# Optimization experiments

Hardware: AMD Instinct MI355X
Metric: run time of the kernel (lower is better)

Reference implementation:

```python
import jax, jax.numpy as jnp
import numpy as np

D_MODEL = 1024
NUM_HEADS = 16
HEAD_DIM = D_MODEL // NUM_HEADS


def setup_inputs() -> dict:
    key = jax.random.key(0)
    ks = jax.random.split(key, 9)
    B, S = 2, 2048
    s = 1.0 / np.sqrt(D_MODEL)
    return {
        "x": jax.random.normal(ks[0], (B, S, D_MODEL), dtype=jnp.float32),
        "Wq": jax.random.normal(ks[1], (D_MODEL, D_MODEL), dtype=jnp.float32) * s,
        "bq": jnp.zeros((D_MODEL,), dtype=jnp.float32),
        "Wk": jax.random.normal(ks[2], (D_MODEL, D_MODEL), dtype=jnp.float32) * s,
        "bk": jnp.zeros((D_MODEL,), dtype=jnp.float32),
        "Wv": jax.random.normal(ks[3], (D_MODEL, D_MODEL), dtype=jnp.float32) * s,
        "bv": jnp.zeros((D_MODEL,), dtype=jnp.float32),
        "Wo": jax.random.normal(ks[4], (D_MODEL, D_MODEL), dtype=jnp.float32) * s,
        "bo": jnp.zeros((D_MODEL,), dtype=jnp.float32),
    }


def reference(x, Wq, bq, Wk, bk, Wv, bv, Wo, bo):
    B, S, _ = x.shape
    # linear projections then split heads: [B, S, D] -> [B, H, S, hd]
    def split_heads(t):
        return t.reshape(B, S, NUM_HEADS, HEAD_DIM).transpose(0, 2, 1, 3)
    q = split_heads(x @ Wq + bq)
    k = split_heads(x @ Wk + bk)
    v = split_heads(x @ Wv + bv)
    # scores: [B, H, S, S]
    scores = jnp.einsum('bhqd,bhkd->bhqk', q, k) / jnp.sqrt(
        jnp.asarray(HEAD_DIM, dtype=x.dtype))
    attn = jax.nn.softmax(scores, axis=-1)
    # dropout is identity in eval mode
    out = jnp.einsum('bhqk,bhkd->bhqd', attn, v)
    out = out.transpose(0, 2, 1, 3).reshape(B, S, D_MODEL)
    return out @ Wo + bo
```

## Files before the change

### kernel.cpp

```cpp
#include <hip/hip_runtime.h>

#define D_MODEL 1024
#define NHEAD 16
#define HD 64
#define BATCH 2
#define SEQ 2048

typedef unsigned short u16;
typedef unsigned int u32;
typedef __bf16 bf16x8 __attribute__((ext_vector_type(8)));
typedef unsigned short u16x8 __attribute__((ext_vector_type(8)));
typedef short s16x4 __attribute__((ext_vector_type(4)));
typedef float f32x4 __attribute__((ext_vector_type(4)));

#if defined(__has_builtin)
#if __has_builtin(__builtin_amdgcn_exp2f)
#define EXP2(x) __builtin_amdgcn_exp2f(x)
#else
#define EXP2(x) exp2f(x)
#endif
#else
#define EXP2(x) exp2f(x)
#endif

static __device__ __forceinline__ u16 f2bf(float f) {
    union { float f; unsigned u; } v; v.f = f;
    unsigned u = v.u;
    u += 0x7fffu + ((u >> 16) & 1u);
    return (u16)(u >> 16);
}

static __device__ __forceinline__ void gld_lds16(const void* g, void* l) {
    __builtin_amdgcn_global_load_lds(
        (const __attribute__((address_space(1))) void*)g,
        (__attribute__((address_space(3))) void*)l, 16, 0, 0);
}

static __device__ __forceinline__ bf16x8 pack_bf8(f32x4 a, f32x4 b) {
    union { float f; unsigned u; } a0, a1, a2, a3, b0, b1, b2, b3;
    a0.f = a[0]; a1.f = a[1]; a2.f = a[2]; a3.f = a[3];
    b0.f = b[0]; b1.f = b[1]; b2.f = b[2]; b3.f = b[3];
    union { unsigned u[4]; bf16x8 v; } r;
    r.u[0] = __builtin_amdgcn_perm(a1.u, a0.u, 0x07060302u);
    r.u[1] = __builtin_amdgcn_perm(a3.u, a2.u, 0x07060302u);
    r.u[2] = __builtin_amdgcn_perm(b1.u, b0.u, 0x07060302u);
    r.u[3] = __builtin_amdgcn_perm(b3.u, b2.u, 0x07060302u);
    return r.v;
}

__global__ __launch_bounds__(256) void k_convert(const float* __restrict__ x,
                                                 const float* __restrict__ wq,
                                                 const float* __restrict__ wk,
                                                 const float* __restrict__ wv,
                                                 const float* __restrict__ wo,
                                                 u16* __restrict__ xb,
                                                 u16* __restrict__ wt) {
    int z = blockIdx.z;
    if (z == 0) {
        int base = (blockIdx.y * 32 + blockIdx.x) * 256 + threadIdx.x;
#pragma unroll
        for (int p = 0; p < 4; p++) {
            int i = base + p * 262144;
            float4 v = ((const float4*)x)[i];
            ushort4 o = make_ushort4(f2bf(v.x), f2bf(v.y), f2bf(v.z), f2bf(v.w));
            ((ushort4*)xb)[i] = o;
        }
        return;
    }
    __shared__ u16 t[32][33];
    const float* W = z == 1 ? wq : z == 2 ? wk : z == 3 ? wv : wo;
    u16* dst = wt + (size_t)(z - 1) * (D_MODEL * D_MODEL);
    int tx = threadIdx.x & 31, ty = threadIdx.x >> 5;
    int n0 = blockIdx.x * 32, k0 = blockIdx.y * 32;
#pragma unroll
    for (int i = 0; i < 4; i++)
        t[ty + i * 8][tx] = f2bf(W[(size_t)(k0 + ty + i * 8) * D_MODEL + n0 + tx]);
    __syncthreads();
#pragma unroll
    for (int i = 0; i < 4; i++)
        dst[(size_t)(n0 + ty + i * 8) * D_MODEL + k0 + tx] = t[tx][ty + i * 8];
}

__global__ __launch_bounds__(256) void k_gemm(const u16* __restrict__ A,
                                              const u16* __restrict__ WtBase,
                                              const float* __restrict__ b0,
                                              const float* __restrict__ b1,
                                              const float* __restrict__ b2,
                                              u16* __restrict__ oq, u16* __restrict__ ok,
                                              u16* __restrict__ ov) {
    __shared__ u16 lA[2 * 128 * 32];
    __shared__ u16 lB[2 * 128 * 32];
    int tid = threadIdx.x, w = tid >> 6, l = tid & 63, lr = l & 15, lq = l >> 4;
    int z = blockIdx.z;
    const u16* Wt = WtBase + (size_t)z * (D_MODEL * D_MODEL);
    const float* bias = z == 0 ? b0 : z == 1 ? b1 : b2;
    float scale = (z == 0) ? (0.125f * 1.44269504088896340736f) : 1.0f;
    int fid2 = blockIdx.y * 8 + blockIdx.x;
    int swz = (fid2 & 7) * 32 + (fid2 >> 3);
    int bx = swz & 7, by = swz >> 3;
    int m0 = by * 128, n0 = bx * 128;
    int wm = (w >> 1) * 64, wn = (w & 1) * 64;
    f32x4 acc[4][4];
#pragma unroll
    for (int mi = 0; mi < 4; mi++)
#pragma unroll
        for (int ni = 0; ni < 4; ni++) acc[mi][ni] = (f32x4){0.f, 0.f, 0.f, 0.f};

    int ra = tid >> 2, ca = (tid & 3) * 8;
    const u16* Aba = A + (size_t)(m0 + ra) * D_MODEL + ca;
    const u16* Abb = A + (size_t)(m0 + 64 + ra) * D_MODEL + ca;
    const u16* Bba = Wt + (size_t)(n0 + ra) * D_MODEL + ca;
    const u16* Bbb = Wt + (size_t)(n0 + 64 + ra) * D_MODEL + ca;

    auto stage = [&](int kk, int buf) {
        gld_lds16(Aba + kk, &lA[buf * 4096 + w * 512]);
        gld_lds16(Abb + kk, &lA[buf * 4096 + 2048 + w * 512]);
        gld_lds16(Bba + kk, &lB[buf * 4096 + w * 512]);
        gld_lds16(Bbb + kk, &lB[buf * 4096 + 2048 + w * 512]);
    };

    stage(0, 0);
    __syncthreads();
    int cur = 0;
    for (int t = 0; t < 32; ++t) {
        if (t + 1 < 32) stage((t + 1) * 32, cur ^ 1);
        bf16x8 af[4], bf[4];
#pragma unroll
        for (int mi = 0; mi < 4; mi++)
            af[mi] = *(const bf16x8*)&lA[cur * 4096 + (wm + mi * 16 + lr) * 32 + lq * 8];
#pragma unroll
        for (int ni = 0; ni < 4; ni++)
            bf[ni] = *(const bf16x8*)&lB[cur * 4096 + (wn + ni * 16 + lr) * 32 + lq * 8];
        __builtin_amdgcn_s_setprio(1);
#pragma unroll
        for (int mi = 0; mi < 4; mi++)
#pragma unroll
            for (int ni = 0; ni < 4; ni++)
                acc[mi][ni] = __builtin_amdgcn_mfma_f32_16x16x32_bf16(
                    af[mi], bf[ni], acc[mi][ni], 0, 0, 0);
        __builtin_amdgcn_s_setprio(0);
        __syncthreads();
        cur ^= 1;
    }
#pragma unroll
    for (int mi = 0; mi < 4; mi++) {
#pragma unroll
        for (int ni = 0; ni < 4; ni++) {
            int col = n0 + wn + ni * 16 + lr;
            float bval = bias[col];
            int row0 = m0 + wm + mi * 16 + lq * 4;
            if (z == 2) {
                int b = row0 >> 11, s = row0 & 2047;
                int h = col >> 6, dd = col & 63;
                ushort4 pk;
                pk.x = f2bf(acc[mi][ni][0] + bval);
                pk.y = f2bf(acc[mi][ni][1] + bval);
                pk.z = f2bf(acc[mi][ni][2] + bval);
                pk.w = f2bf(acc[mi][ni][3] + bval);
                *(ushort4*)&ov[((size_t)(b * NHEAD + h) * HD + dd) * SEQ + s] = pk;
            } else {
#pragma unroll
                for (int r = 0; r < 4; r++) {
                    int row = row0 + r;
                    float val = (acc[mi][ni][r] + bval) * scale;
                    u16* op = z == 0 ? oq : ok;
                    int b = row >> 11, s = row & 2047, h = col >> 6, d = col & 63;
                    op[(((size_t)(b * NHEAD + h)) * SEQ + s) * HD + d] = f2bf(val);
                }
            }
        }
    }
}

__global__ __launch_bounds__(256) void k_gout(const u16* __restrict__ A,
                                              const u16* __restrict__ Wt,
                                              const float* __restrict__ bias,
                                              float* __restrict__ outf) {
    __shared__ u16 lA[2 * 64 * 32];
    __shared__ u16 lB[2 * 64 * 32];
    int tid = threadIdx.x, w = tid >> 6, l = tid & 63, lr = l & 15, lq = l >> 4;
    int fid = blockIdx.y * 16 + blockIdx.x;
    int swz = (fid & 7) * 128 + (fid >> 3);
    int bx = swz & 15, by = swz >> 4;
    int m0 = by * 64, n0 = bx * 64;
    int wm = (w >> 1) * 32, wn = (w & 1) * 32;
    f32x4 acc[2][2];
#pragma unroll
    for (int mi = 0; mi < 2; mi++)
#pragma unroll
        for (int ni = 0; ni < 2; ni++) acc[mi][ni] = (f32x4){0.f, 0.f, 0.f, 0.f};

    int ra = tid >> 2, ca = (tid & 3) * 8;
    const u16* Aba = A + (size_t)(m0 + ra) * D_MODEL + ca;
    const u16* Bba = Wt + (size_t)(n0 + ra) * D_MODEL + ca;

    auto stage = [&](int kk, int buf) {
        gld_lds16(Aba + kk, &lA[buf * 2048 + w * 512]);
        gld_lds16(Bba + kk, &lB[buf * 2048 + w * 512]);
    };

    stage(0, 0);
    __syncthreads();
    int cur = 0;
    for (int t = 0; t < 32; ++t) {
        if (t + 1 < 32) stage((t + 1) * 32, cur ^ 1);
        bf16x8 af[2], bf[2];
#pragma unroll
        for (int mi = 0; mi < 2; mi++)
            af[mi] = *(const bf16x8*)&lA[cur * 2048 + (wm + mi * 16 + lr) * 32 + lq * 8];
#pragma unroll
        for (int ni = 0; ni < 2; ni++)
            bf[ni] = *(const bf16x8*)&lB[cur * 2048 + (wn + ni * 16 + lr) * 32 + lq * 8];
        __builtin_amdgcn_s_setprio(1);
#pragma unroll
        for (int mi = 0; mi < 2; mi++)
#pragma unroll
            for (int ni = 0; ni < 2; ni++)
                acc[mi][ni] = __builtin_amdgcn_mfma_f32_16x16x32_bf16(
                    af[mi], bf[ni], acc[mi][ni], 0, 0, 0);
        __builtin_amdgcn_s_setprio(0);
        __syncthreads();
        cur ^= 1;
    }
#pragma unroll
    for (int mi = 0; mi < 2; mi++)
#pragma unroll
        for (int ni = 0; ni < 2; ni++) {
            int col = n0 + wn + ni * 16 + lr;
            float bval = bias[col];
#pragma unroll
            for (int r = 0; r < 4; r++) {
                int row = m0 + wm + mi * 16 + lq * 4 + r;
                outf[(size_t)row * D_MODEL + col] = acc[mi][ni][r] + bval;
            }
        }
}

static __device__ __forceinline__ int ksw(int row, int col) {
    return row * 64 + ((((col >> 3) ^ (row & 7)) << 3) | (col & 7));
}
static __device__ __forceinline__ int vsw(int row, int col) {
    return row * 128 + ((((col >> 3) ^ (row & 15)) << 3) | (col & 7));
}

__global__ __launch_bounds__(256) void k_attn(const u16* __restrict__ Q,
                                              const u16* __restrict__ K,
                                              const u16* __restrict__ VT,
                                              u16* __restrict__ part0,
                                              u16* __restrict__ part1,
                                              float* __restrict__ lsum, int nsplit) {
    __shared__ __align__(16) u16 lK[128 * 64];
    __shared__ __align__(16) u16 lVt[64 * 128];
    int tid = threadIdx.x, w = tid >> 6, l = tid & 63, lr = l & 15, lq = l >> 4;
    int bl = blockIdx.x;
    int qt = bl / (32 * nsplit);
    int rem = bl - qt * (32 * nsplit);
    int bh = rem / nsplit;
    int ks = rem - bh * nsplit;
    int qb = qt * 128 + w * 32;
    const u16* Qb = Q + (size_t)bh * SEQ * HD;
    const u16* Kb = K + (size_t)bh * SEQ * HD;
    const u16* VTb = VT + (size_t)bh * HD * SEQ;

    bf16x8 qf[2][2];
#pragma unroll
    for (int tq = 0; tq < 2; tq++)
#pragma unroll
        for (int kc = 0; kc < 2; kc++)
            qf[tq][kc] = *(const bf16x8*)&Qb[(size_t)(qb + tq * 16 + lr) * HD +
                                             kc * 32 + lq * 8];
    f32x4 o[2][4];
    f32x4 ol[2];
#pragma unroll
    for (int tq = 0; tq < 2; tq++) {
        ol[tq] = (f32x4){0.f, 0.f, 0.f, 0.f};
#pragma unroll
        for (int di = 0; di < 4; di++) o[tq][di] = (f32x4){0.f, 0.f, 0.f, 0.f};
    }
    union { u16 s[8]; bf16x8 v; } onev;
#pragma unroll
    for (int i = 0; i < 8; i++) onev.s[i] = 0x3F80;
    const bf16x8 vone8 = onev.v;

    int krow = tid >> 3, kch = tid & 7;
    int vrow = tid >> 4, vch = tid & 15;

    int nk = SEQ / nsplit;
    int jbeg = ks * nk, jend = jbeg + nk;

    u16x8 kreg[4], vreg[4];
#pragma unroll
    for (int p = 0; p < 4; p++) {
        kreg[p] = *(const u16x8*)&Kb[(size_t)(jbeg + p * 32 + krow) * HD + kch * 8];
        vreg[p] = *(const u16x8*)&VTb[(size_t)(p * 16 + vrow) * SEQ + jbeg + vch * 8];
    }

    for (int j0 = jbeg; j0 < jend; j0 += 128) {
        __syncthreads();
#pragma unroll
        for (int p = 0; p < 4; p++) {
            *(u16x8*)&lK[ksw(p * 32 + krow, kch * 8)] = kreg[p];
            *(u16x8*)&lVt[vsw(p * 16 + vrow, vch * 8)] = vreg[p];
        }
        __syncthreads();
        if (j0 + 128 < jend) {
            int jn = j0 + 128;
#pragma unroll
            for (int p = 0; p < 4; p++) {
                kreg[p] = *(const u16x8*)&Kb[(size_t)(jn + p * 32 + krow) * HD + kch * 8];
                vreg[p] = *(const u16x8*)&VTb[(size_t)(p * 16 + vrow) * SEQ + jn + vch * 8];
            }
        }

#pragma unroll
        for (int kh = 0; kh < 2; kh++) {
#pragma unroll
            for (int t2 = 0; t2 < 2; t2++) {
                int rA = kh * 64 + t2 * 32 + lr;
                int rB = rA + 16;
                bf16x8 kA0 = *(const bf16x8*)&lK[ksw(rA, lq * 8)];
                bf16x8 kA1 = *(const bf16x8*)&lK[ksw(rA, 32 + lq * 8)];
                bf16x8 kB0 = *(const bf16x8*)&lK[ksw(rB, lq * 8)];
                bf16x8 kB1 = *(const bf16x8*)&lK[ksw(rB, 32 + lq * 8)];
                f32x4 sA0 = (f32x4){0.f, 0.f, 0.f, 0.f};
                f32x4 sA1 = (f32x4){0.f, 0.f, 0.f, 0.f};
                f32x4 sB0 = (f32x4){0.f, 0.f, 0.f, 0.f};
                f32x4 sB1 = (f32x4){0.f, 0.f, 0.f, 0.f};
                __builtin_amdgcn_s_setprio(1);
                sA0 = __builtin_amdgcn_mfma_f32_16x16x32_bf16(kA0, qf[0][0], sA0, 0, 0, 0);
                sB0 = __builtin_amdgcn_mfma_f32_16x16x32_bf16(kB0, qf[0][0], sB0, 0, 0, 0);
                sA1 = __builtin_amdgcn_mfma_f32_16x16x32_bf16(kA0, qf[1][0], sA1, 0, 0, 0);
                sB1 = __builtin_amdgcn_mfma_f32_16x16x32_bf16(kB0, qf[1][0], sB1, 0, 0, 0);
                sA0 = __builtin_amdgcn_mfma_f32_16x16x32_bf16(kA1, qf[0][1], sA0, 0, 0, 0);
                sB0 = __builtin_amdgcn_mfma_f32_16x16x32_bf16(kB1, qf[0][1], sB0, 0, 0, 0);
                sA1 = __builtin_amdgcn_mfma_f32_16x16x32_bf16(kA1, qf[1][1], sA1, 0, 0, 0);
                sB1 = __builtin_amdgcn_mfma_f32_16x16x32_bf16(kB1, qf[1][1], sB1, 0, 0, 0);
                __builtin_amdgcn_s_setprio(0);
#pragma unroll
                for (int r = 0; r < 4; r++) {
                    sA0[r] = EXP2(sA0[r]);
                    sA1[r] = EXP2(sA1[r]);
                    sB0[r] = EXP2(sB0[r]);
                    sB1[r] = EXP2(sB1[r]);
                }
                bf16x8 pf0 = pack_bf8(sA0, sB0);
                bf16x8 pf1 = pack_bf8(sA1, sB1);
                __builtin_amdgcn_s_setprio(1);
                ol[0] = __builtin_amdgcn_mfma_f32_16x16x32_bf16(pf0, vone8, ol[0], 0, 0, 0);
                ol[1] = __builtin_amdgcn_mfma_f32_16x16x32_bf16(pf1, vone8, ol[1], 0, 0, 0);
#pragma unroll
                for (int di = 0; di < 4; di++) {
                    int vr = di * 16 + lr;
                    union { bf16x8 v; s16x4 h[2]; } vv;
                    vv.h[0] = *(const s16x4*)&lVt[vsw(vr, kh * 64 + t2 * 32 + lq * 4)];
                    vv.h[1] = *(const s16x4*)&lVt[vsw(vr, kh * 64 + t2 * 32 + 16 + lq * 4)];
                    o[0][di] = __builtin_amdgcn_mfma_f32_16x16x32_bf16(pf0, vv.v,
                                                                       o[0][di], 0, 0, 0);
                    o[1][di] = __builtin_amdgcn_mfma_f32_16x16x32_bf16(pf1, vv.v,
                                                                       o[1][di], 0, 0, 0);
                }
                __builtin_amdgcn_s_setprio(0);
            }
        }
    }
    int b = bh >> 4, h = bh & 15;
    if (nsplit == 1) {
#pragma unroll
        for (int tq = 0; tq < 2; tq++) {
#pragma unroll
            for (int di = 0; di < 4; di++)
#pragma unroll
                for (int r = 0; r < 4; r++) {
                    int qg = qb + tq * 16 + lq * 4 + r;
                    part0[((size_t)(b * SEQ + qg)) * D_MODEL + h * 64 + di * 16 + lr] =
                        f2bf(o[tq][di][r] / ol[tq][r]);
                }
        }
    } else {
        u16* pdst = (ks == 0) ? part0 : part1;
#pragma unroll
        for (int tq = 0; tq < 2; tq++)
#pragma unroll
            for (int di = 0; di < 4; di++)
#pragma unroll
                for (int r = 0; r < 4; r++) {
                    int qg = qb + tq * 16 + lq * 4 + r;
                    union { _Float16 h; u16 u; } cv;
                    cv.h = (_Float16)o[tq][di][r];
                    pdst[((size_t)(b * SEQ + qg)) * D_MODEL + h * 64 + di * 16 + lr] =
                        cv.u;
                }
        if (lr == 0) {
#pragma unroll
            for (int tq = 0; tq < 2; tq++)
#pragma unroll
                for (int r = 0; r < 4; r++) {
                    int qg = qb + tq * 16 + lq * 4 + r;
                    lsum[(ks * 32 + bh) * 2048 + qg] = ol[tq][r];
                }
        }
    }
}

__global__ __launch_bounds__(256) void k_combine(const u16* __restrict__ p0,
                                                 const u16* __restrict__ p1,
                                                 const float* __restrict__ lsum,
                                                 u16* __restrict__ dst) {
    int i = blockIdx.x * 256 + threadIdx.x;
    size_t a8 = (size_t)i * 8;
    int row = (int)(a8 >> 10);
    int col = (int)(a8 & 1023);
    int b = row >> 11, q = row & 2047, h = col >> 6;
    int mi = ((b << 4) + h) * 2048 + q;
    float inv = 1.0f / (lsum[mi] + lsum[65536 + mi]);
    u16x8 h0 = *(const u16x8*)(p0 + a8);
    u16x8 h1 = *(const u16x8*)(p1 + a8);
    u16x8 out;
#pragma unroll
    for (int j = 0; j < 8; j++) {
        union { _Float16 h; u16 u; } c0, c1;
        c0.u = h0[j]; c1.u = h1[j];
        out[j] = f2bf(((float)c0.h + (float)c1.h) * inv);
    }
    *(u16x8*)(dst + a8) = out;
}

extern "C" void kernel_launch(void* const* d_in, const int* in_sizes, int n_in,
                              void* d_out, int out_size, void* d_ws, size_t ws_size,
                              hipStream_t stream) {
    const float* x  = (const float*)d_in[0];
    const float* Wq = (const float*)d_in[1];
    const float* bq = (const float*)d_in[2];
    const float* Wk = (const float*)d_in[3];
    const float* bk = (const float*)d_in[4];
    const float* Wv = (const float*)d_in[5];
    const float* bv = (const float*)d_in[6];
    const float* Wo = (const float*)d_in[7];
    const float* bo = (const float*)d_in[8];
    float* out = (float*)d_out;

    char* ws = (char*)d_ws;
    u16* xb  = (u16*)ws;
    u16* wt  = (u16*)(ws + (size_t)8 * 1024 * 1024);
    u16* qws = (u16*)(ws + (size_t)16 * 1024 * 1024);
    u16* kws = (u16*)(ws + (size_t)24 * 1024 * 1024);
    u16* vtw = (u16*)(ws + (size_t)32 * 1024 * 1024);
    u16* ao  = (u16*)(ws + (size_t)40 * 1024 * 1024);
    float* ml = (float*)(ws + (size_t)48 * 1024 * 1024);

    int nsplit = (ws_size >= (size_t)49 * 1024 * 1024) ? 2 : 1;
    u16* attn_out = (nsplit == 2) ? xb : ao;

    k_convert<<<dim3(32, 32, 5), 256, 0, stream>>>(x, Wq, Wk, Wv, Wo, xb, wt);
    k_gemm<<<dim3(8, 32, 3), 256, 0, stream>>>(xb, wt, bq, bk, bv, qws, kws, vtw);
    if (nsplit == 2) {
        k_attn<<<16 * 32 * 2, 256, 0, stream>>>(qws, kws, vtw, xb, ao, ml, 2);
        k_combine<<<2048, 256, 0, stream>>>(xb, ao, ml, xb);
    } else {
        k_attn<<<16 * 32, 256, 0, stream>>>(qws, kws, vtw, ao, nullptr, ml, 1);
    }
    k_gout<<<dim3(16, 64), 256, 0, stream>>>(attn_out,
                                             wt + (size_t)3 * D_MODEL * D_MODEL,
                                             bo, out);
}
```

Measured before the change: 190.1 us.

## Software-pipeline QK^T with exp/PV in attention and permute V layout

Restructures the attention inner loop so the QK^T MFMAs for the next 32-key sub-tile are issued before the exp and PV MFMAs of the current one, using double-buffered score registers. The V projection epilogue now writes V^T with a permuted sequence index within 32-element groups, so each lane can load a contiguous 8-element V fragment with one 16-byte LDS read instead of two 8-byte reads. It also adds a launch bound of 4 blocks per SM and removes the setprio hints. The intent is to overlap the exp latency with matrix work and cut LDS instructions, at the cost of more live registers, which the occupancy bound may force into spills.

```diff
diff --git a/kernel.cpp b/kernel.cpp
--- a/kernel.cpp
+++ b/kernel.cpp
@@ -152,12 +152,13 @@
             if (z == 2) {
                 int b = row0 >> 11, s = row0 & 2047;
                 int h = col >> 6, dd = col & 63;
+                int sp = (s & ~31) | ((s & 12) << 1) | ((s & 16) >> 2);
                 ushort4 pk;
                 pk.x = f2bf(acc[mi][ni][0] + bval);
                 pk.y = f2bf(acc[mi][ni][1] + bval);
                 pk.z = f2bf(acc[mi][ni][2] + bval);
                 pk.w = f2bf(acc[mi][ni][3] + bval);
-                *(ushort4*)&ov[((size_t)(b * NHEAD + h) * HD + dd) * SEQ + s] = pk;
+                *(ushort4*)&ov[((size_t)(b * NHEAD + h) * HD + dd) * SEQ + sp] = pk;
             } else {
 #pragma unroll
                 for (int r = 0; r < 4; r++) {
@@ -243,12 +244,12 @@
     return row * 128 + ((((col >> 3) ^ (row & 15)) << 3) | (col & 7));
 }
 
-__global__ __launch_bounds__(256) void k_attn(const u16* __restrict__ Q,
-                                              const u16* __restrict__ K,
-                                              const u16* __restrict__ VT,
-                                              u16* __restrict__ part0,
-                                              u16* __restrict__ part1,
-                                              float* __restrict__ lsum, int nsplit) {
+__global__ __launch_bounds__(256, 4) void k_attn(const u16* __restrict__ Q,
+                                                 const u16* __restrict__ K,
+                                                 const u16* __restrict__ VT,
+                                                 u16* __restrict__ part0,
+                                                 u16* __restrict__ part1,
+                                                 float* __restrict__ lsum, int nsplit) {
     __shared__ __align__(16) u16 lK[128 * 64];
     __shared__ __align__(16) u16 lVt[64 * 128];
     int tid = threadIdx.x, w = tid >> 6, l = tid & 63, lr = l & 15, lq = l >> 4;
@@ -295,6 +296,26 @@
         vreg[p] = *(const u16x8*)&VTb[(size_t)(p * 16 + vrow) * SEQ + jbeg + vch * 8];
     }
 
+    bf16x8 kf[2][4];
+    f32x4 sc[2][4];
+    auto krdqk = [&](int u, int ss) {
+        int rA = u * 32 + lr, rB = rA + 16;
+        kf[ss][0] = *(const bf16x8*)&lK[ksw(rA, lq * 8)];
+        kf[ss][1] = *(const bf16x8*)&lK[ksw(rA, 32 + lq * 8)];
+        kf[ss][2] = *(const bf16x8*)&lK[ksw(rB, lq * 8)];
+        kf[ss][3] = *(const bf16x8*)&lK[ksw(rB, 32 + lq * 8)];
+#pragma unroll
+        for (int j = 0; j < 4; j++) sc[ss][j] = (f32x4){0.f, 0.f, 0.f, 0.f};
+        sc[ss][0] = __builtin_amdgcn_mfma_f32_16x16x32_bf16(kf[ss][0], qf[0][0], sc[ss][0], 0, 0, 0);
+        sc[ss][2] = __builtin_amdgcn_mfma_f32_16x16x32_bf16(kf[ss][2], qf[0][0], sc[ss][2], 0, 0, 0);
+        sc[ss][1] = __builtin_amdgcn_mfma_f32_16x16x32_bf16(kf[ss][0], qf[1][0], sc[ss][1], 0, 0, 0);
+        sc[ss][3] = __builtin_amdgcn_mfma_f32_16x16x32_bf16(kf[ss][2], qf[1][0], sc[ss][3], 0, 0, 0);
+        sc[ss][0] = __builtin_amdgcn_mfma_f32_16x16x32_bf16(kf[ss][1], qf[0][1], sc[ss][0], 0, 0, 0);
+        sc[ss][2] = __builtin_amdgcn_mfma_f32_16x16x32_bf16(kf[ss][3], qf[0][1], sc[ss][2], 0, 0, 0);
+        sc[ss][1] = __builtin_amdgcn_mfma_f32_16x16x32_bf16(kf[ss][1], qf[1][1], sc[ss][1], 0, 0, 0);
+        sc[ss][3] = __builtin_amdgcn_mfma_f32_16x16x32_bf16(kf[ss][3], qf[1][1], sc[ss][3], 0, 0, 0);
+    };
+
     for (int j0 = jbeg; j0 < jend; j0 += 128) {
         __syncthreads();
 #pragma unroll
@@ -312,54 +333,33 @@
             }
         }
 
-#pragma unroll
-        for (int kh = 0; kh < 2; kh++) {
-#pragma unroll
-            for (int t2 = 0; t2 < 2; t2++) {
-                int rA = kh * 64 + t2 * 32 + lr;
-                int rB = rA + 16;
-                bf16x8 kA0 = *(const bf16x8*)&lK[ksw(rA, lq * 8)];
-                bf16x8 kA1 = *(const bf16x8*)&lK[ksw(rA, 32 + lq * 8)];
-                bf16x8 kB0 = *(const bf16x8*)&lK[ksw(rB, lq * 8)];
-                bf16x8 kB1 = *(const bf16x8*)&lK[ksw(rB, 32 + lq * 8)];
-                f32x4 sA0 = (f32x4){0.f, 0.f, 0.f, 0.f};
-                f32x4 sA1 = (f32x4){0.f, 0.f, 0.f, 0.f};
-                f32x4 sB0 = (f32x4){0.f, 0.f, 0.f, 0.f};
-                f32x4 sB1 = (f32x4){0.f, 0.f, 0.f, 0.f};
-                __builtin_amdgcn_s_setprio(1);
-                sA0 = __builtin_amdgcn_mfma_f32_16x16x32_bf16(kA0, qf[0][0], sA0, 0, 0, 0);
-                sB0 = __builtin_amdgcn_mfma_f32_16x16x32_bf16(kB0, qf[0][0], sB0, 0, 0, 0);
-                sA1 = __builtin_amdgcn_mfma_f32_16x16x32_bf16(kA0, qf[1][0], sA1, 0, 0, 0);
-                sB1 = __builtin_amdgcn_mfma_f32_16x16x32_bf16(kB0, qf[1][0], sB1, 0, 0, 0);
-                sA0 = __builtin_amdgcn_mfma_f32_16x16x32_bf16(kA1, qf[0][1], sA0, 0, 0, 0);
-                sB0 = __builtin_amdgcn_mfma_f32_16x16x32_bf16(kB1, qf[0][1], sB0, 0, 0, 0);
-                sA1 = __builtin_amdgcn_mfma_f32_16x16x32_bf16(kA1, qf[1][1], sA1, 0, 0, 0);
-                sB1 = __builtin_amdgcn_mfma_f32_16x16x32_bf16(kB1, qf[1][1], sB1, 0, 0, 0);
-                __builtin_amdgcn_s_setprio(0);
-#pragma unroll
-                for (int r = 0; r < 4; r++) {
-                    sA0[r] = EXP2(sA0[r]);
-                    sA1[r] = EXP2(sA1[r]);
-                    sB0[r] = EXP2(sB0[r]);
-                    sB1[r] = EXP2(sB1[r]);
-                }
-                bf16x8 pf0 = pack_bf8(sA0, sB0);
-                bf16x8 pf1 = pack_bf8(sA1, sB1);
-                __builtin_amdgcn_s_setprio(1);
-                ol[0] = __builtin_amdgcn_mfma_f32_16x16x32_bf16(pf0, vone8, ol[0], 0, 0, 0);
-                ol[1] = __builtin_amdgcn_mfma_f32_16x16x32_bf16(pf1, vone8, ol[1], 0, 0, 0);
-#pragma unroll
-                for (int di = 0; di < 4; di++) {
-                    int vr = di * 16 + lr;
-                    union { bf16x8 v; s16x4 h[2]; } vv;
-                    vv.h[0] = *(const s16x4*)&lVt[vsw(vr, kh * 64 + t2 * 32 + lq * 4)];
-                    vv.h[1] = *(const s16x4*)&lVt[vsw(vr, kh * 64 + t2 * 32 + 16 + lq * 4)];
-                    o[0][di] = __builtin_amdgcn_mfma_f32_16x16x32_bf16(pf0, vv.v,
-                                                                       o[0][di], 0, 0, 0);
-                    o[1][di] = __builtin_amdgcn_mfma_f32_16x16x32_bf16(pf1, vv.v,
-                                                                       o[1][di], 0, 0, 0);
-                }
-                __builtin_amdgcn_s_setprio(0);
+        krdqk(0, 0);
+#pragma unroll
+        for (int u = 0; u < 4; ++u) {
+            if (u < 3) krdqk(u + 1, (u + 1) & 1);
+            bf16x8 vv[4];
+#pragma unroll
+            for (int di = 0; di < 4; di++)
+                vv[di] = *(const bf16x8*)&lVt[vsw(di * 16 + lr, u * 32 + lq * 8)];
+            f32x4 e0 = sc[u & 1][0], e1 = sc[u & 1][1];
+            f32x4 e2 = sc[u & 1][2], e3 = sc[u & 1][3];
+#pragma unroll
+            for (int r = 0; r < 4; r++) {
+                e0[r] = EXP2(e0[r]);
+                e1[r] = EXP2(e1[r]);
+                e2[r] = EXP2(e2[r]);
+                e3[r] = EXP2(e3[r]);
+            }
+            bf16x8 pf0 = pack_bf8(e0, e2);
+            bf16x8 pf1 = pack_bf8(e1, e3);
+            ol[0] = __builtin_amdgcn_mfma_f32_16x16x32_bf16(pf0, vone8, ol[0], 0, 0, 0);
+            ol[1] = __builtin_amdgcn_mfma_f32_16x16x32_bf16(pf1, vone8, ol[1], 0, 0, 0);
+#pragma unroll
+            for (int di = 0; di < 4; di++) {
+                o[0][di] = __builtin_amdgcn_mfma_f32_16x16x32_bf16(pf0, vv[di],
+                                                                   o[0][di], 0, 0, 0);
+                o[1][di] = __builtin_amdgcn_mfma_f32_16x16x32_bf16(pf1, vv[di],
+                                                                   o[1][di], 0, 0, 0);
             }
         }
     }
```

Result: slower. 205.4 us (+8.1%).
